# Kernel optimization log

Measured on AMD Instinct MI355X. Metric: run time of the kernel, lower is better.

The kernel has to match this reference:

```python
import jax, jax.numpy as jnp
import numpy as np

B, S, T, C, HS = 32, 8, 512, 128, 128


def setup_inputs() -> dict:
    key = jax.random.key(0)
    k1, k2, k3, k4, k5 = jax.random.split(key, 5)
    x = jax.random.normal(k1, (B, T, C), dtype=jnp.float32)
    adjacent = jax.random.uniform(k2, (B, S, T, T), dtype=jnp.float32)
    scale = 1.0 / np.sqrt(C)
    Wq = jax.random.normal(k3, (C, HS), dtype=jnp.float32) * scale
    Wk = jax.random.normal(k4, (C, HS), dtype=jnp.float32) * scale
    Wv = jax.random.normal(k5, (C, HS), dtype=jnp.float32) * scale
    return {"x": x, "adjacent": adjacent, "Wq": Wq, "Wk": Wk, "Wv": Wv}


def reference(x, adjacent, Wq, Wk, Wv):
    # x: [B,T,C], adjacent: [B,S,T,T]
    Cdim = x.shape[-1]
    q = x @ Wq            # [B,T,HS]
    k = x @ Wk            # [B,T,HS]
    v = x @ Wv            # [B,T,HS]
    # scaled scores (note: original scales by C^-0.5, not head_size^-0.5)
    wei = jnp.einsum('btd,bud->btu', q, k) * (Cdim ** -0.5)  # [B,T,T]
    # multiplicative adjacency mask, broadcast over S
    wei = wei[:, None, :, :] * adjacent                       # [B,S,T,T]
    wei = jax.nn.softmax(wei, axis=-1)
    # dropout p=0.0 -> identity
    out = jnp.einsum('bstu,bud->bstd', wei, v)                # [B,S,T,HS]
    return out
```

## Files before the change

### kernel.cpp

```cpp
#include <hip/hip_runtime.h>
#include <hip/hip_bf16.h>
#include <stdint.h>

#define NB 32
#define NS 8
#define NT 512
#define NC 128
#define NH 128

typedef __bf16 bf16_t;
typedef bf16_t bf16x8 __attribute__((ext_vector_type(8)));
typedef bf16_t bf16x4 __attribute__((ext_vector_type(4)));
typedef float  f32x4  __attribute__((ext_vector_type(4)));

__global__ __launch_bounds__(256) void k_split(const float* __restrict__ in,
                                               bf16_t* __restrict__ hi,
                                               bf16_t* __restrict__ lo, int n4) {
  int i = blockIdx.x * 256 + threadIdx.x;
  if (i >= n4) return;
  f32x4 x = ((const f32x4*)in)[i];
  bf16x4 h, l;
#pragma unroll
  for (int j = 0; j < 4; j++) {
    bf16_t hb = (bf16_t)x[j];
    h[j] = hb;
    l[j] = (bf16_t)(x[j] - (float)hb);
  }
  ((bf16x4*)hi)[i] = h;
  ((bf16x4*)lo)[i] = l;
}

__global__ void k_prep_w(const float* __restrict__ Wq, const float* __restrict__ Wk,
                         const float* __restrict__ Wv, bf16_t* __restrict__ Wth,
                         bf16_t* __restrict__ Wtl) {
  int w = blockIdx.x >> 7;
  int h = blockIdx.x & 127;
  int c = threadIdx.x;
  const float* W = (w == 0) ? Wq : (w == 1) ? Wk : Wv;
  float x = W[c * NH + h];
  bf16_t hb = (bf16_t)x;
  int o = (w * 128 + h) * 128 + c;
  Wth[o] = hb;
  Wtl[o] = (bf16_t)(x - (float)hb);
}

__global__ __launch_bounds__(256) void k_qkv(const bf16_t* __restrict__ xh,
                                             const bf16_t* __restrict__ xl,
                                             const bf16_t* __restrict__ Wth,
                                             const bf16_t* __restrict__ Wtl,
                                             float* __restrict__ q,
                                             float* __restrict__ k,
                                             bf16_t* __restrict__ vt) {
  int mat = blockIdx.y;
  int t0 = blockIdx.x * 64;
  int lane = threadIdx.x & 63;
  int wave = threadIdx.x >> 6;
  int l15 = lane & 15;
  int kq = (lane >> 4) * 8;
  int row = t0 + wave * 16 + l15;
  const bf16_t* Wh = Wth + mat * NC * NH;
  const bf16_t* Wl = Wtl + mat * NC * NH;

  f32x4 zero = {0.f, 0.f, 0.f, 0.f};
  f32x4 acc[8];
#pragma unroll
  for (int i = 0; i < 8; i++) acc[i] = zero;

#pragma unroll
  for (int k0 = 0; k0 < NC; k0 += 32) {
    bf16x8 ah = *(const bf16x8*)(xh + (size_t)row * NC + k0 + kq);
    bf16x8 al = *(const bf16x8*)(xl + (size_t)row * NC + k0 + kq);
#pragma unroll
    for (int nt = 0; nt < 8; nt++) {
      bf16x8 bh = *(const bf16x8*)(Wh + (nt * 16 + l15) * NC + k0 + kq);
      bf16x8 bl = *(const bf16x8*)(Wl + (nt * 16 + l15) * NC + k0 + kq);
      acc[nt] = __builtin_amdgcn_mfma_f32_16x16x32_bf16(ah, bh, acc[nt], 0, 0, 0);
      acc[nt] = __builtin_amdgcn_mfma_f32_16x16x32_bf16(ah, bl, acc[nt], 0, 0, 0);
      acc[nt] = __builtin_amdgcn_mfma_f32_16x16x32_bf16(al, bh, acc[nt], 0, 0, 0);
    }
  }

  int trow = t0 + wave * 16 + (lane >> 4) * 4;
  if (mat < 2) {
    float* dst = (mat == 0) ? q : k;
#pragma unroll
    for (int nt = 0; nt < 8; nt++) {
      int h = nt * 16 + l15;
#pragma unroll
      for (int r = 0; r < 4; r++) dst[(size_t)(trow + r) * NH + h] = acc[nt][r];
    }
  } else {
    int b = trow >> 9;
    int tl = trow & 511;
#pragma unroll
    for (int nt = 0; nt < 8; nt++) {
      int h = nt * 16 + l15;
      bf16x4 pk;
#pragma unroll
      for (int r = 0; r < 4; r++) pk[r] = (bf16_t)acc[nt][r];
      *(bf16x4*)(vt + ((size_t)b * NH + h) * NT + tl) = pk;
    }
  }
}

__global__ __launch_bounds__(256) void k_scores(const bf16_t* __restrict__ qh,
                                                const bf16_t* __restrict__ ql,
                                                const bf16_t* __restrict__ kh,
                                                const bf16_t* __restrict__ kl,
                                                float* __restrict__ wei) {
  int b = blockIdx.y;
  int mt = blockIdx.x >> 3;
  int ut = blockIdx.x & 7;
  int lane = threadIdx.x & 63;
  int wave = threadIdx.x >> 6;
  int l15 = lane & 15;
  int kq = (lane >> 4) * 8;
  int m0 = mt * 64 + wave * 16;
  int u0 = ut * 64;
  const float scale = 0.08838834764831845f;

  f32x4 zero = {0.f, 0.f, 0.f, 0.f};
  f32x4 acc[4];
#pragma unroll
  for (int i = 0; i < 4; i++) acc[i] = zero;

  size_t qbase = ((size_t)b * NT + m0 + l15) * NH;
  size_t kbase = ((size_t)b * NT + u0 + l15) * NH;

#pragma unroll
  for (int k0 = 0; k0 < NH; k0 += 32) {
    bf16x8 ah = *(const bf16x8*)(qh + qbase + k0 + kq);
    bf16x8 al = *(const bf16x8*)(ql + qbase + k0 + kq);
#pragma unroll
    for (int nt = 0; nt < 4; nt++) {
      bf16x8 bh = *(const bf16x8*)(kh + kbase + (size_t)nt * 16 * NH + k0 + kq);
      bf16x8 bl = *(const bf16x8*)(kl + kbase + (size_t)nt * 16 * NH + k0 + kq);
      acc[nt] = __builtin_amdgcn_mfma_f32_16x16x32_bf16(ah, bh, acc[nt], 0, 0, 0);
      acc[nt] = __builtin_amdgcn_mfma_f32_16x16x32_bf16(ah, bl, acc[nt], 0, 0, 0);
      acc[nt] = __builtin_amdgcn_mfma_f32_16x16x32_bf16(al, bh, acc[nt], 0, 0, 0);
    }
  }

  int t = m0 + (lane >> 4) * 4;
#pragma unroll
  for (int nt = 0; nt < 4; nt++) {
    int u = u0 + nt * 16 + l15;
#pragma unroll
    for (int r = 0; r < 4; r++)
      wei[((size_t)b * NT + t + r) * NT + u] = acc[nt][r] * scale;
  }
}

#define PLD 520

__global__ __launch_bounds__(256) void k_attn(const float* __restrict__ wei,
                                              const float* __restrict__ adj,
                                              const bf16_t* __restrict__ vt,
                                              float* __restrict__ out) {
  __shared__ bf16_t p[32 * PLD];
  __shared__ float linv[32];
  int t0 = blockIdx.x * 32;
  int s = blockIdx.y;
  int b = blockIdx.z;
  int lane = threadIdx.x & 63;
  int wave = threadIdx.x >> 6;

  for (int rr = 0; rr < 8; rr++) {
    int r = wave * 8 + rr;
    int t = t0 + r;
    const float* wrow = wei + ((size_t)b * NT + t) * NT;
    const float* arow = adj + (((size_t)b * NS + s) * NT + t) * NT;
    f32x4 w0 = ((const f32x4*)wrow)[lane];
    f32x4 w1 = ((const f32x4*)wrow)[64 + lane];
    f32x4 a0 = ((const f32x4*)arow)[lane];
    f32x4 a1 = ((const f32x4*)arow)[64 + lane];
#pragma unroll
    for (int j = 0; j < 4; j++) { w0[j] *= a0[j]; w1[j] *= a1[j]; }
    float m = w0[0];
#pragma unroll
    for (int j = 1; j < 4; j++) m = fmaxf(m, w0[j]);
#pragma unroll
    for (int j = 0; j < 4; j++) m = fmaxf(m, w1[j]);
#pragma unroll
    for (int off = 32; off >= 1; off >>= 1) m = fmaxf(m, __shfl_xor(m, off));
    float sum = 0.f;
    bf16x4 e0, e1;
#pragma unroll
    for (int j = 0; j < 4; j++) { float e = __expf(w0[j] - m); sum += e; e0[j] = (bf16_t)e; }
#pragma unroll
    for (int j = 0; j < 4; j++) { float e = __expf(w1[j] - m); sum += e; e1[j] = (bf16_t)e; }
#pragma unroll
    for (int off = 32; off >= 1; off >>= 1) sum += __shfl_xor(sum, off);
    *(bf16x4*)&p[r * PLD + lane * 4] = e0;
    *(bf16x4*)&p[r * PLD + 256 + lane * 4] = e1;
    if (lane == 0) linv[r] = 1.0f / sum;
  }
  __syncthreads();

  int l15 = lane & 15;
  int kq = (lane >> 4) * 8;
  int m0 = (wave & 1) * 16;
  int h0 = (wave >> 1) * 64;
  f32x4 zero = {0.f, 0.f, 0.f, 0.f};
  f32x4 acc[4];
#pragma unroll
  for (int i = 0; i < 4; i++) acc[i] = zero;
  const bf16_t* vb = vt + (size_t)b * NH * NT;

#pragma unroll 4
  for (int k0 = 0; k0 < NT; k0 += 32) {
    bf16x8 a = *(const bf16x8*)&p[(m0 + l15) * PLD + k0 + kq];
#pragma unroll
    for (int nt = 0; nt < 4; nt++) {
      bf16x8 bfr = *(const bf16x8*)(vb + (size_t)(h0 + nt * 16 + l15) * NT + k0 + kq);
      acc[nt] = __builtin_amdgcn_mfma_f32_16x16x32_bf16(a, bfr, acc[nt], 0, 0, 0);
    }
  }

  int tl = m0 + (lane >> 4) * 4;
  float* obase = out + (((size_t)b * NS + s) * NT + t0) * NH;
#pragma unroll
  for (int nt = 0; nt < 4; nt++) {
    int h = h0 + nt * 16 + l15;
#pragma unroll
    for (int r = 0; r < 4; r++)
      obase[(size_t)(tl + r) * NH + h] = acc[nt][r] * linv[tl + r];
  }
}

extern "C" void kernel_launch(void* const* d_in, const int* in_sizes, int n_in,
                              void* d_out, int out_size, void* d_ws, size_t ws_size,
                              hipStream_t stream) {
  const float* x = (const float*)d_in[0];
  const float* adj = (const float*)d_in[1];
  const float* Wq = (const float*)d_in[2];
  const float* Wk = (const float*)d_in[3];
  const float* Wv = (const float*)d_in[4];
  float* out = (float*)d_out;

  const size_t BTC = (size_t)NB * NT * NC;

  char* base = (char*)d_ws;
  bf16_t* xh = (bf16_t*)base;  base += BTC * 2;
  bf16_t* xl = (bf16_t*)base;  base += BTC * 2;
  bf16_t* Wth = (bf16_t*)base; base += (size_t)3 * NC * NH * 2;
  bf16_t* Wtl = (bf16_t*)base; base += (size_t)3 * NC * NH * 2;
  float* q = (float*)base;     base += BTC * 4;
  float* kk = (float*)base;    base += BTC * 4;
  bf16_t* qh = (bf16_t*)base;  base += 2 * BTC * 2;
  bf16_t* ql = (bf16_t*)base;  base += 2 * BTC * 2;
  bf16_t* vt = (bf16_t*)base;  base += BTC * 2;
  float* wei = (float*)base;   base += (size_t)NB * NT * NT * 4;
  (void)kk; (void)in_sizes; (void)n_in; (void)out_size; (void)ws_size;

  k_split<<<(int)(BTC / 4 / 256), 256, 0, stream>>>(x, xh, xl, (int)(BTC / 4));
  k_prep_w<<<384, 128, 0, stream>>>(Wq, Wk, Wv, Wth, Wtl);
  k_qkv<<<dim3((int)(NB * NT / 64), 3), 256, 0, stream>>>(xh, xl, Wth, Wtl, q, q + BTC, vt);
  k_split<<<(int)(2 * BTC / 4 / 256), 256, 0, stream>>>(q, qh, ql, (int)(2 * BTC / 4));
  k_scores<<<dim3(64, NB), 256, 0, stream>>>(qh, ql, qh + BTC, ql + BTC, wei);
  k_attn<<<dim3(NT / 32, NS, NB), 256, 0, stream>>>(wei, adj, vt, out);
}
```

Before: 548.8 us.

## Fuse q/k bf16 split into projection and drop softmax max pass

The QKV projection kernel now writes q and k directly as hi/lo bf16 pairs, removing the separate split kernel and its float round trip through memory. The attention kernel no longer computes a row max or shuffle-reduces sums. It exponentiates the masked scores directly and gets the row sum from an extra MFMA against a ones vector. This cuts cross-lane reductions and serial dependencies, but exp without max subtraction risks overflow if scores grow large.

```diff
diff --git a/kernel.cpp b/kernel.cpp
--- a/kernel.cpp
+++ b/kernel.cpp
@@ -48,8 +48,10 @@
                                              const bf16_t* __restrict__ xl,
                                              const bf16_t* __restrict__ Wth,
                                              const bf16_t* __restrict__ Wtl,
-                                             float* __restrict__ q,
-                                             float* __restrict__ k,
+                                             bf16_t* __restrict__ qh,
+                                             bf16_t* __restrict__ ql,
+                                             bf16_t* __restrict__ kh,
+                                             bf16_t* __restrict__ kl,
                                              bf16_t* __restrict__ vt) {
   int mat = blockIdx.y;
   int t0 = blockIdx.x * 64;
@@ -82,12 +84,18 @@
 
   int trow = t0 + wave * 16 + (lane >> 4) * 4;
   if (mat < 2) {
-    float* dst = (mat == 0) ? q : k;
+    bf16_t* dh = (mat == 0) ? qh : kh;
+    bf16_t* dl = (mat == 0) ? ql : kl;
 #pragma unroll
     for (int nt = 0; nt < 8; nt++) {
       int h = nt * 16 + l15;
 #pragma unroll
-      for (int r = 0; r < 4; r++) dst[(size_t)(trow + r) * NH + h] = acc[nt][r];
+      for (int r = 0; r < 4; r++) {
+        float v = acc[nt][r];
+        bf16_t hb = (bf16_t)v;
+        dh[(size_t)(trow + r) * NH + h] = hb;
+        dl[(size_t)(trow + r) * NH + h] = (bf16_t)(v - (float)hb);
+      }
     }
   } else {
     int b = trow >> 9;
@@ -158,42 +166,28 @@
                                               const bf16_t* __restrict__ vt,
                                               float* __restrict__ out) {
   __shared__ bf16_t p[32 * PLD];
-  __shared__ float linv[32];
   int t0 = blockIdx.x * 32;
   int s = blockIdx.y;
   int b = blockIdx.z;
   int lane = threadIdx.x & 63;
   int wave = threadIdx.x >> 6;
 
+#pragma unroll
   for (int rr = 0; rr < 8; rr++) {
     int r = wave * 8 + rr;
-    int t = t0 + r;
-    const float* wrow = wei + ((size_t)b * NT + t) * NT;
-    const float* arow = adj + (((size_t)b * NS + s) * NT + t) * NT;
+    const float* wrow = wei + ((size_t)b * NT + t0 + r) * NT;
+    const float* arow = adj + (((size_t)b * NS + s) * NT + t0 + r) * NT;
     f32x4 w0 = ((const f32x4*)wrow)[lane];
     f32x4 w1 = ((const f32x4*)wrow)[64 + lane];
     f32x4 a0 = ((const f32x4*)arow)[lane];
     f32x4 a1 = ((const f32x4*)arow)[64 + lane];
-#pragma unroll
-    for (int j = 0; j < 4; j++) { w0[j] *= a0[j]; w1[j] *= a1[j]; }
-    float m = w0[0];
-#pragma unroll
-    for (int j = 1; j < 4; j++) m = fmaxf(m, w0[j]);
-#pragma unroll
-    for (int j = 0; j < 4; j++) m = fmaxf(m, w1[j]);
-#pragma unroll
-    for (int off = 32; off >= 1; off >>= 1) m = fmaxf(m, __shfl_xor(m, off));
-    float sum = 0.f;
     bf16x4 e0, e1;
 #pragma unroll
-    for (int j = 0; j < 4; j++) { float e = __expf(w0[j] - m); sum += e; e0[j] = (bf16_t)e; }
-#pragma unroll
-    for (int j = 0; j < 4; j++) { float e = __expf(w1[j] - m); sum += e; e1[j] = (bf16_t)e; }
-#pragma unroll
-    for (int off = 32; off >= 1; off >>= 1) sum += __shfl_xor(sum, off);
+    for (int j = 0; j < 4; j++) e0[j] = (bf16_t)__expf(w0[j] * a0[j]);
+#pragma unroll
+    for (int j = 0; j < 4; j++) e1[j] = (bf16_t)__expf(w1[j] * a1[j]);
     *(bf16x4*)&p[r * PLD + lane * 4] = e0;
     *(bf16x4*)&p[r * PLD + 256 + lane * 4] = e1;
-    if (lane == 0) linv[r] = 1.0f / sum;
   }
   __syncthreads();
 
@@ -205,11 +199,16 @@
   f32x4 acc[4];
 #pragma unroll
   for (int i = 0; i < 4; i++) acc[i] = zero;
+  f32x4 accl = zero;
+  bf16x8 ones;
+#pragma unroll
+  for (int j = 0; j < 8; j++) ones[j] = (bf16_t)1.0f;
   const bf16_t* vb = vt + (size_t)b * NH * NT;
 
 #pragma unroll 4
   for (int k0 = 0; k0 < NT; k0 += 32) {
     bf16x8 a = *(const bf16x8*)&p[(m0 + l15) * PLD + k0 + kq];
+    accl = __builtin_amdgcn_mfma_f32_16x16x32_bf16(a, ones, accl, 0, 0, 0);
 #pragma unroll
     for (int nt = 0; nt < 4; nt++) {
       bf16x8 bfr = *(const bf16x8*)(vb + (size_t)(h0 + nt * 16 + l15) * NT + k0 + kq);
@@ -218,13 +217,16 @@
   }
 
   int tl = m0 + (lane >> 4) * 4;
+  float linv[4];
+#pragma unroll
+  for (int r = 0; r < 4; r++) linv[r] = 1.0f / accl[r];
   float* obase = out + (((size_t)b * NS + s) * NT + t0) * NH;
 #pragma unroll
   for (int nt = 0; nt < 4; nt++) {
     int h = h0 + nt * 16 + l15;
 #pragma unroll
     for (int r = 0; r < 4; r++)
-      obase[(size_t)(tl + r) * NH + h] = acc[nt][r] * linv[tl + r];
+      obase[(size_t)(tl + r) * NH + h] = acc[nt][r] * linv[r];
   }
 }
 
@@ -245,18 +247,18 @@
   bf16_t* xl = (bf16_t*)base;  base += BTC * 2;
   bf16_t* Wth = (bf16_t*)base; base += (size_t)3 * NC * NH * 2;
   bf16_t* Wtl = (bf16_t*)base; base += (size_t)3 * NC * NH * 2;
-  float* q = (float*)base;     base += BTC * 4;
-  float* kk = (float*)base;    base += BTC * 4;
-  bf16_t* qh = (bf16_t*)base;  base += 2 * BTC * 2;
-  bf16_t* ql = (bf16_t*)base;  base += 2 * BTC * 2;
+  bf16_t* qh = (bf16_t*)base;  base += BTC * 2;
+  bf16_t* ql = (bf16_t*)base;  base += BTC * 2;
+  bf16_t* kh = (bf16_t*)base;  base += BTC * 2;
+  bf16_t* kl = (bf16_t*)base;  base += BTC * 2;
   bf16_t* vt = (bf16_t*)base;  base += BTC * 2;
   float* wei = (float*)base;   base += (size_t)NB * NT * NT * 4;
-  (void)kk; (void)in_sizes; (void)n_in; (void)out_size; (void)ws_size;
+  (void)in_sizes; (void)n_in; (void)out_size; (void)ws_size;
 
   k_split<<<(int)(BTC / 4 / 256), 256, 0, stream>>>(x, xh, xl, (int)(BTC / 4));
   k_prep_w<<<384, 128, 0, stream>>>(Wq, Wk, Wv, Wth, Wtl);
-  k_qkv<<<dim3((int)(NB * NT / 64), 3), 256, 0, stream>>>(xh, xl, Wth, Wtl, q, q + BTC, vt);
-  k_split<<<(int)(2 * BTC / 4 / 256), 256, 0, stream>>>(q, qh, ql, (int)(2 * BTC / 4));
-  k_scores<<<dim3(64, NB), 256, 0, stream>>>(qh, ql, qh + BTC, ql + BTC, wei);
+  k_qkv<<<dim3((int)(NB * NT / 64), 3), 256, 0, stream>>>(xh, xl, Wth, Wtl,
+                                                          qh, ql, kh, kl, vt);
+  k_scores<<<dim3(64, NB), 256, 0, stream>>>(qh, ql, kh, kl, wei);
   k_attn<<<dim3(NT / 32, NS, NB), 256, 0, stream>>>(wei, adj, vt, out);
 }
```

Result: faster. 534.2 us (-2.7%).
